# Kernel optimization log

Hardware: AMD Instinct MI355X
Metric: run time of the kernel (lower is better)

Reference implementation:

```python
import jax, jax.numpy as jnp
import numpy as np

N_LAGS = 64
EPS = 1e-8


def setup_inputs() -> dict:
    key = jax.random.key(0)
    x = jax.random.normal(key, (16, 8, 250, 1024), dtype=jnp.float32)
    return {"x": x}


def reference(x):
    B, M, T, L = x.shape
    # rfft over all mics once (shared across pairs)
    X = jnp.fft.rfft(x, axis=-1)  # [B, M, T, L//2+1] complex
    # all mic pairs (m1 < m2), row-major order matching the torch double loop
    i1, i2 = np.triu_indices(M, k=1)
    X1 = X[:, i1]  # [B, P, T, F]
    X2 = X[:, i2]  # [B, P, T, F]
    R = X1 * jnp.conj(X2)
    R = R / (jnp.abs(R) + EPS)  # PHAT weighting
    cc = jnp.fft.irfft(R, n=L, axis=-1)        # [B, P, T, L]
    cc = jnp.fft.fftshift(cc, axes=-1)
    center = L // 2
    start = center - N_LAGS // 2
    return cc[..., start:start + N_LAGS]        # [B, P, T, n_lags]
```

## Files before the change

### kernel.cpp

```cpp
#include <hip/hip_runtime.h>
#include <math.h>

#define B_    16
#define M_    8
#define T_    250
#define L_    1024
#define NPAIR 28

#define KTOT   1024
#define CH_K   256
#define NKT    8
#define NCHUNK 4
#define APITCH 264

typedef _Float16 half8  __attribute__((ext_vector_type(8)));
typedef _Float16 half2t __attribute__((ext_vector_type(2)));
typedef float    floatx4 __attribute__((ext_vector_type(4)));

__device__ __align__(16) _Float16 g_Btw[64 * KTOT];

__constant__ int c_i1[NPAIR] = {0,0,0,0,0,0,0,1,1,1,1,1,1,2,2,2,2,2,3,3,3,3,4,4,4,5,5,6};
__constant__ int c_i2[NPAIR] = {1,2,3,4,5,6,7,2,3,4,5,6,7,3,4,5,6,7,4,5,6,7,5,6,7,6,7,7};

__global__ void init_btw() {
    int idx = blockIdx.x * 256 + threadIdx.x;
    int n = idx >> 10, k = idx & 1023;
    float v;
    if (k == 0)      v = 1.0f / 1024.0f;
    else if (k == 1) v = (n & 1) ? (-1.0f / 1024.0f) : (1.0f / 1024.0f);
    else {
        int bin = k >> 1, tau = n - 32;
        int r = (tau * bin) & 1023;
        float ang = (float)r * (6.283185307179586f / 1024.0f);
        float s, c; sincosf(ang, &s, &c);
        v = ((k & 1) ? -s : c) * (2.0f / 1024.0f);
    }
    g_Btw[idx] = (_Float16)v;
}

#define PHI(i) ((i) ^ (((i) >> 4) & 15) ^ ((((i) >> 8) & 3) << 1))

__device__ inline float2 cmul(float2 a, float2 b) {
    return make_float2(fmaf(a.x, b.x, -a.y * b.y), fmaf(a.x, b.y, a.y * b.x));
}
__device__ inline float2 cadd(float2 a, float2 b) { return make_float2(a.x + b.x, a.y + b.y); }
__device__ inline float2 csub(float2 a, float2 b) { return make_float2(a.x - b.x, a.y - b.y); }
__device__ inline float2 cmni(float2 a) { return make_float2(a.y, -a.x); }

__device__ inline void dft8(float2 v[8]) {
    const float rt = 0.70710678118654752440f;
    float2 b0 = cadd(v[0], v[4]), b1 = cadd(v[1], v[5]);
    float2 b2 = cadd(v[2], v[6]), b3 = cadd(v[3], v[7]);
    float2 c0 = csub(v[0], v[4]);
    float2 t1 = csub(v[1], v[5]);
    float2 c1 = make_float2(rt * (t1.x + t1.y), rt * (t1.y - t1.x));
    float2 c2 = cmni(csub(v[2], v[6]));
    float2 t3 = csub(v[3], v[7]);
    float2 c3 = make_float2(rt * (t3.y - t3.x), -rt * (t3.x + t3.y));
    float2 f0 = cadd(b0, b2), f1 = cadd(b1, b3);
    float2 g0 = csub(b0, b2), g1 = cmni(csub(b1, b3));
    v[0] = cadd(f0, f1); v[4] = csub(f0, f1);
    v[2] = cadd(g0, g1); v[6] = csub(g0, g1);
    f0 = cadd(c0, c2); f1 = cadd(c1, c3);
    g0 = csub(c0, c2); g1 = cmni(csub(c1, c3));
    v[1] = cadd(f0, f1); v[5] = csub(f0, f1);
    v[3] = cadd(g0, g1); v[7] = csub(g0, g1);
}

__device__ inline void twiddle8(float2 v[8], float2 w1) {
    float2 w2 = cmul(w1, w1);
    float2 w3 = cmul(w2, w1);
    float2 w4 = cmul(w2, w2);
    float2 w5 = cmul(w4, w1);
    float2 w6 = cmul(w4, w2);
    float2 w7 = cmul(w4, w3);
    v[1] = cmul(v[1], w1); v[2] = cmul(v[2], w2); v[3] = cmul(v[3], w3);
    v[4] = cmul(v[4], w4); v[5] = cmul(v[5], w5); v[6] = cmul(v[6], w6);
    v[7] = cmul(v[7], w7);
}

__device__ inline int posmap(int k) {
    return ((k & 1) << 9) | (((k >> 1) & 7) << 6) | (((k >> 4) & 7) << 3) | ((k >> 7) & 7);
}

__global__ __launch_bounds__(512, 4) void gcc_main(const float* __restrict__ x,
                                                   float* __restrict__ out) {
    __shared__ float2 s_z[4 * 1024];
    __shared__ __align__(16) _Float16 sA[32 * APITCH];

    const int tid = threadIdx.x;
    const int t = blockIdx.x, b = blockIdx.y;
    const int f = tid & 127, c = tid >> 7;
    float2* Zb = s_z + c * 1024;

    float ws, wc;
    sincosf((float)f * (-6.283185307179586f / 1024.0f), &ws, &wc);
    const float2 w = make_float2(wc, ws);

    {
        const float* xa = x + (((size_t)b * M_ + 2 * c) * T_ + t) * L_;
        const float* xb = xa + (size_t)T_ * L_;
        float va[8], vb[8];
#pragma unroll
        for (int j = 0; j < 8; ++j) { va[j] = xa[f + 128 * j]; vb[j] = xb[f + 128 * j]; }
        const float rt = 0.70710678118654752440f;
#pragma unroll
        for (int q = 0; q < 4; ++q) {
            float2 a = make_float2(va[q], vb[q]);
            float2 d = make_float2(va[q + 4], vb[q + 4]);
            float2 tq = cmul(csub(a, d), w);
            float2 r;
            if (q == 0)      r = tq;
            else if (q == 1) r = make_float2(rt * (tq.x + tq.y), rt * (tq.y - tq.x));
            else if (q == 2) r = make_float2(tq.y, -tq.x);
            else             r = make_float2(rt * (tq.y - tq.x), -rt * (tq.x + tq.y));
            Zb[PHI(f + 128 * q)]       = cadd(a, d);
            Zb[PHI(f + 128 * q + 512)] = r;
        }
    }
    __syncthreads();

    {
        float2 wl = w;
        if (f & 64) wl = cmul(wl, make_float2(0.92387953251128674f, 0.38268343236508977f));
        const float2 wB = cmul(wl, wl);
        const int base = (f >> 6) * 512 + (f & 63);
        float2 v[8];
#pragma unroll
        for (int r = 0; r < 8; ++r) v[r] = Zb[PHI(base + 64 * r)];
        dft8(v);
        twiddle8(v, wB);
#pragma unroll
        for (int k = 0; k < 8; ++k) Zb[PHI(base + 64 * k)] = v[k];
    }
    __syncthreads();

    {
        float s2, c2;
        sincosf((float)(f & 7) * (-6.283185307179586f / 64.0f), &s2, &c2);
        const float2 wC = make_float2(c2, s2);
        const int base = (f >> 3) * 64 + (f & 7);
        float2 v[8];
#pragma unroll
        for (int r = 0; r < 8; ++r) v[r] = Zb[PHI(base + 8 * r)];
        dft8(v);
        twiddle8(v, wC);
#pragma unroll
        for (int k = 0; k < 8; ++k) Zb[PHI(base + 8 * k)] = v[k];
    }
    __syncthreads();

    {
        const int base = f * 8;
        float2 v[8];
#pragma unroll
        for (int r = 0; r < 8; ++r) v[r] = Zb[PHI(base + r)];
        dft8(v);
#pragma unroll
        for (int k = 0; k < 8; ++k) Zb[PHI(base + k)] = v[k];
    }
    __syncthreads();

    const int lane = tid & 63, wv = tid >> 6;
    const int mt = wv >> 2, nt = wv & 3;
    const int l15 = lane & 15, quad = lane >> 4;
    const int arow = mt * 16 + l15;
    const _Float16* Bbase = g_Btw + (nt * 16 + l15) * KTOT;
    floatx4 acc = {0.0f, 0.0f, 0.0f, 0.0f};

    const int bl = tid & 127, pg = tid >> 7;

#define PAIRA(p_, a_, b_)                                                     \
    {                                                                         \
        float2 X1 = Xs[a_], X2 = Xs[b_];                                      \
        float rr = X1.x * X2.x + X1.y * X2.y;                                 \
        float ri = X1.y * X2.x - X1.x * X2.y;                                 \
        float m2 = rr * rr + ri * ri;                                         \
        float inv = (m2 > 1e-30f) ? rsqrtf(m2) : 0.0f;                        \
        *(half2t*)&sA[(p_) * APITCH + 2 * bl] =                               \
            (half2t){(_Float16)(rr * inv), (_Float16)(ri * inv)};             \
    }

    auto fillA = [&](int h) {
        const int beta = h * 128 + bl;
        const int pa = posmap(beta);
        const int pb = posmap((1024 - beta) & 1023);
        float2 Xs[8];
#pragma unroll
        for (int cc = 0; cc < 4; ++cc) {
            float2 Aa = s_z[cc * 1024 + PHI(pa)];
            float2 Bb = s_z[cc * 1024 + PHI(pb)];
            Xs[2 * cc]     = make_float2(0.5f * (Aa.x + Bb.x), 0.5f * (Aa.y - Bb.y));
            Xs[2 * cc + 1] = make_float2(0.5f * (Aa.y + Bb.y), 0.5f * (Bb.x - Aa.x));
        }
        if (pg == 0) {
            PAIRA(0, 0, 1) PAIRA(1, 0, 2) PAIRA(2, 0, 3) PAIRA(3, 0, 4)
            PAIRA(4, 0, 5) PAIRA(5, 0, 6) PAIRA(6, 0, 7)
        } else if (pg == 1) {
            PAIRA(7, 1, 2) PAIRA(8, 1, 3) PAIRA(9, 1, 4) PAIRA(10, 1, 5)
            PAIRA(11, 1, 6) PAIRA(12, 1, 7) PAIRA(13, 2, 3)
        } else if (pg == 2) {
            PAIRA(14, 2, 4) PAIRA(15, 2, 5) PAIRA(16, 2, 6) PAIRA(17, 2, 7)
            PAIRA(18, 3, 4) PAIRA(19, 3, 5) PAIRA(20, 3, 6)
        } else {
            PAIRA(21, 3, 7) PAIRA(22, 4, 5) PAIRA(23, 4, 6) PAIRA(24, 4, 7)
            PAIRA(25, 5, 6) PAIRA(26, 5, 7) PAIRA(27, 6, 7)
        }
        if (h == 0 && bl == 0) {
            const int pN = 4;
#pragma unroll
            for (int pp = 0; pp < 7; ++pp) {
                const int p = pg * 7 + pp;
                float2 Za = s_z[(c_i1[p] >> 1) * 1024 + pN];
                float2 Zc = s_z[(c_i2[p] >> 1) * 1024 + pN];
                float x1 = (c_i1[p] & 1) ? Za.y : Za.x;
                float x2 = (c_i2[p] & 1) ? Zc.y : Zc.x;
                float rr = x1 * x2;
                float inv = (rr * rr > 1e-30f) ? rsqrtf(rr * rr) : 0.0f;
                sA[p * APITCH + 1] = (_Float16)(rr * inv);
            }
        }
    };

    for (int h = 0; h < NCHUNK; ++h) {
        fillA(h);
        __syncthreads();

        const _Float16* Ap = sA + arow * APITCH;
        const _Float16* Bp = Bbase + h * CH_K;
#pragma unroll
        for (int kt = 0; kt < NKT; ++kt) {
            half8 af = *(const half8*)(Ap + kt * 32 + quad * 8);
            half8 bf = *(const half8*)(Bp + kt * 32 + quad * 8);
            acc = __builtin_amdgcn_mfma_f32_16x16x32_f16(af, bf, acc, 0, 0, 0);
        }
        __syncthreads();
    }

#pragma unroll
    for (int r = 0; r < 4; ++r) {
        int pair = mt * 16 + quad * 4 + r;
        if (pair < NPAIR)
            out[((((size_t)b * NPAIR + pair) * T_ + t) << 6) + nt * 16 + l15] = acc[r];
    }
}

extern "C" void kernel_launch(void* const* d_in, const int* in_sizes, int n_in,
                              void* d_out, int out_size, void* d_ws, size_t ws_size,
                              hipStream_t stream) {
    (void)in_sizes; (void)n_in; (void)d_ws; (void)ws_size; (void)out_size;
    hipLaunchKernelGGL(init_btw, dim3(256), dim3(256), 0, stream);
    hipLaunchKernelGGL(gcc_main, dim3(T_, B_), dim3(512), 0, stream,
                       (const float*)d_in[0], (float*)d_out);
}
```

Before: 296.6 us.

## Alias FFT scratch with fp16 spectrum and A tile in shared memory

After the FFT, a new pass unpacks the two-real-channel spectra once per bin into a compact fp16 interleaved buffer, with the Nyquist bin stored separately. The FFT scratch array is then reused for that buffer and for the A tile through a shared-memory union, which shrinks per-block LDS. The smaller LDS footprint is meant to let more blocks fit per CU, and fillA now does one vector load per bin instead of gathered float2 loads with arithmetic. In exchange it adds an extra barrier pass and rounds the spectrum to fp16 before PHAT normalisation.

```diff
diff --git a/kernel.cpp b/kernel.cpp
--- a/kernel.cpp
+++ b/kernel.cpp
@@ -12,6 +12,7 @@
 #define NKT    8
 #define NCHUNK 4
 #define APITCH 264
+#define XPLANE (516 * 8)
 
 typedef _Float16 half8  __attribute__((ext_vector_type(8)));
 typedef _Float16 half2t __attribute__((ext_vector_type(2)));
@@ -83,15 +84,22 @@
     return ((k & 1) << 9) | (((k >> 1) & 7) << 6) | (((k >> 4) & 7) << 3) | ((k >> 7) & 7);
 }
 
+union SMem {
+    float2 z[4 * 1024];
+    struct {
+        _Float16 X[2 * XPLANE];
+        _Float16 A[32 * APITCH];
+    } p;
+};
+
 __global__ __launch_bounds__(512, 4) void gcc_main(const float* __restrict__ x,
                                                    float* __restrict__ out) {
-    __shared__ float2 s_z[4 * 1024];
-    __shared__ __align__(16) _Float16 sA[32 * APITCH];
+    __shared__ __align__(16) SMem sm;
 
     const int tid = threadIdx.x;
     const int t = blockIdx.x, b = blockIdx.y;
     const int f = tid & 127, c = tid >> 7;
-    float2* Zb = s_z + c * 1024;
+    float2* Zb = sm.z + c * 1024;
 
     float ws, wc;
     sincosf((float)f * (-6.283185307179586f / 1024.0f), &ws, &wc);
@@ -161,6 +169,56 @@
     }
     __syncthreads();
 
+    {
+        const int k = tid;
+        const int pa = posmap(k);
+        const int pb = posmap((1024 - k) & 1023);
+        float2 Z8[8];
+#pragma unroll
+        for (int cc = 0; cc < 4; ++cc) {
+            Z8[2 * cc]     = sm.z[cc * 1024 + PHI(pa)];
+            Z8[2 * cc + 1] = sm.z[cc * 1024 + PHI(pb)];
+        }
+        float2 ny0 = make_float2(0.f, 0.f), ny1 = ny0, ny2 = ny0, ny3 = ny0;
+        if (tid == 0) {
+            ny0 = sm.z[0 * 1024 + 4]; ny1 = sm.z[1 * 1024 + 4];
+            ny2 = sm.z[2 * 1024 + 4]; ny3 = sm.z[3 * 1024 + 4];
+        }
+        __syncthreads();
+
+        half8 lo, hi;
+#pragma unroll
+        for (int cc = 0; cc < 4; ++cc) {
+            float2 Aa = Z8[2 * cc], Bb = Z8[2 * cc + 1];
+            float xr = Aa.x + Bb.x, xi = Aa.y - Bb.y;
+            float yr = Aa.y + Bb.y, yi = Bb.x - Aa.x;
+            const int o = (cc & 1) * 4;
+            if (cc < 2) {
+                lo[o + 0] = (_Float16)xr; lo[o + 1] = (_Float16)xi;
+                lo[o + 2] = (_Float16)yr; lo[o + 3] = (_Float16)yi;
+            } else {
+                hi[o + 0] = (_Float16)xr; hi[o + 1] = (_Float16)xi;
+                hi[o + 2] = (_Float16)yr; hi[o + 3] = (_Float16)yi;
+            }
+        }
+        *(half8*)(sm.p.X + 0 * XPLANE + k * 8) = lo;
+        *(half8*)(sm.p.X + 1 * XPLANE + k * 8) = hi;
+        if (tid == 0) {
+            half8 nlo, nhi;
+            nlo[0] = (_Float16)ny0.x; nlo[1] = (_Float16)0.f;
+            nlo[2] = (_Float16)ny0.y; nlo[3] = (_Float16)0.f;
+            nlo[4] = (_Float16)ny1.x; nlo[5] = (_Float16)0.f;
+            nlo[6] = (_Float16)ny1.y; nlo[7] = (_Float16)0.f;
+            nhi[0] = (_Float16)ny2.x; nhi[1] = (_Float16)0.f;
+            nhi[2] = (_Float16)ny2.y; nhi[3] = (_Float16)0.f;
+            nhi[4] = (_Float16)ny3.x; nhi[5] = (_Float16)0.f;
+            nhi[6] = (_Float16)ny3.y; nhi[7] = (_Float16)0.f;
+            *(half8*)(sm.p.X + 0 * XPLANE + 512 * 8) = nlo;
+            *(half8*)(sm.p.X + 1 * XPLANE + 512 * 8) = nhi;
+        }
+        __syncthreads();
+    }
+
     const int lane = tid & 63, wv = tid >> 6;
     const int mt = wv >> 2, nt = wv & 3;
     const int l15 = lane & 15, quad = lane >> 4;
@@ -177,21 +235,19 @@
         float ri = X1.y * X2.x - X1.x * X2.y;                                 \
         float m2 = rr * rr + ri * ri;                                         \
         float inv = (m2 > 1e-30f) ? rsqrtf(m2) : 0.0f;                        \
-        *(half2t*)&sA[(p_) * APITCH + 2 * bl] =                               \
+        *(half2t*)&sm.p.A[(p_) * APITCH + 2 * bl] =                           \
             (half2t){(_Float16)(rr * inv), (_Float16)(ri * inv)};             \
     }
 
     auto fillA = [&](int h) {
-        const int beta = h * 128 + bl;
-        const int pa = posmap(beta);
-        const int pb = posmap((1024 - beta) & 1023);
+        const int bin = h * 128 + bl;
+        half8 lo = *(const half8*)(sm.p.X + 0 * XPLANE + bin * 8);
+        half8 hi = *(const half8*)(sm.p.X + 1 * XPLANE + bin * 8);
         float2 Xs[8];
 #pragma unroll
-        for (int cc = 0; cc < 4; ++cc) {
-            float2 Aa = s_z[cc * 1024 + PHI(pa)];
-            float2 Bb = s_z[cc * 1024 + PHI(pb)];
-            Xs[2 * cc]     = make_float2(0.5f * (Aa.x + Bb.x), 0.5f * (Aa.y - Bb.y));
-            Xs[2 * cc + 1] = make_float2(0.5f * (Aa.y + Bb.y), 0.5f * (Bb.x - Aa.x));
+        for (int ch = 0; ch < 4; ++ch) {
+            Xs[ch]     = make_float2((float)lo[2 * ch], (float)lo[2 * ch + 1]);
+            Xs[4 + ch] = make_float2((float)hi[2 * ch], (float)hi[2 * ch + 1]);
         }
         if (pg == 0) {
             PAIRA(0, 0, 1) PAIRA(1, 0, 2) PAIRA(2, 0, 3) PAIRA(3, 0, 4)
@@ -207,17 +263,15 @@
             PAIRA(25, 5, 6) PAIRA(26, 5, 7) PAIRA(27, 6, 7)
         }
         if (h == 0 && bl == 0) {
-            const int pN = 4;
 #pragma unroll
             for (int pp = 0; pp < 7; ++pp) {
                 const int p = pg * 7 + pp;
-                float2 Za = s_z[(c_i1[p] >> 1) * 1024 + pN];
-                float2 Zc = s_z[(c_i2[p] >> 1) * 1024 + pN];
-                float x1 = (c_i1[p] & 1) ? Za.y : Za.x;
-                float x2 = (c_i2[p] & 1) ? Zc.y : Zc.x;
+                const int ca = c_i1[p], cb = c_i2[p];
+                float x1 = (float)sm.p.X[(ca >> 2) * XPLANE + 512 * 8 + (ca & 3) * 2];
+                float x2 = (float)sm.p.X[(cb >> 2) * XPLANE + 512 * 8 + (cb & 3) * 2];
                 float rr = x1 * x2;
                 float inv = (rr * rr > 1e-30f) ? rsqrtf(rr * rr) : 0.0f;
-                sA[p * APITCH + 1] = (_Float16)(rr * inv);
+                sm.p.A[p * APITCH + 1] = (_Float16)(rr * inv);
             }
         }
     };
@@ -226,7 +280,7 @@
         fillA(h);
         __syncthreads();
 
-        const _Float16* Ap = sA + arow * APITCH;
+        const _Float16* Ap = sm.p.A + arow * APITCH;
         const _Float16* Bp = Bbase + h * CH_K;
 #pragma unroll
         for (int kt = 0; kt < NKT; ++kt) {
```

After: 288.3 us. 1.03x faster.
